# Performance work log

Hardware: AMD Instinct MI355X
Metric: run time of the kernel (lower is better)

The kernel has to match this reference:

```python
import jax, jax.numpy as jnp
import numpy as np

_CLIP_MIN = 1e-06
_POS_ALPHA = 0.001
NUM_CLASSES = 26
RADIUS = 3
POOL = 3  # rmi_pool_size == rmi_pool_stride
HALF_D = RADIUS * RADIUS


def _max_pool2d(x):
    # torch F.max_pool2d(kernel=3, stride=3, padding=1): pads with -inf
    return jax.lax.reduce_window(
        x, -jnp.inf, jax.lax.max,
        window_dimensions=(1, 1, POOL, POOL),
        window_strides=(1, 1, POOL, POOL),
        padding=[(0, 0), (0, 0), (1, 1), (1, 1)])


def _get_pairs(x):
    # stack radius^2 shifted views: [n,c,H,W] -> [n,c,half_d,new_h,new_w]
    h, w = x.shape[2], x.shape[3]
    nh, nw = h - (RADIUS - 1), w - (RADIUS - 1)
    views = [x[:, :, y:y + nh, xx:xx + nw] for y in range(RADIUS) for xx in range(RADIUS)]
    return jnp.stack(views, axis=2)


def _log_det_by_cholesky(m):
    chol = jnp.linalg.cholesky(m)
    diag = jnp.diagonal(chol, axis1=-2, axis2=-1)
    return 2.0 * jnp.sum(jnp.log(diag + 1e-08), axis=-1)


def _rmi_lower_bound(labels_4D, probs_4D):
    labels_4D = _max_pool2d(labels_4D)
    probs_4D = _max_pool2d(probs_4D)
    n, c = labels_4D.shape[0], labels_4D.shape[1]
    la = _get_pairs(labels_4D).reshape(n, c, HALF_D, -1)  # [n,c,9,M]
    pr = _get_pairs(probs_4D).reshape(n, c, HALF_D, -1)
    eye = jnp.eye(HALF_D, dtype=pr.dtype)
    la = la - jnp.mean(la, axis=3, keepdims=True)
    pr = pr - jnp.mean(pr, axis=3, keepdims=True)
    la_cov = jnp.einsum('ncdm,ncem->ncde', la, la)
    pr_cov = jnp.einsum('ncdm,ncem->ncde', pr, pr)
    pr_cov_inv = jnp.linalg.inv(pr_cov + eye * _POS_ALPHA)
    la_pr_cov = jnp.einsum('ncdm,ncem->ncde', la, pr)
    appro_var = la_cov - jnp.einsum('ncde,ncef,ncgf->ncdg', la_pr_cov, pr_cov_inv, la_pr_cov)
    rmi_now = 0.5 * _log_det_by_cholesky(appro_var + eye * _POS_ALPHA)  # [n,c]
    rmi_per_class = jnp.mean(rmi_now.reshape(-1, NUM_CLASSES), axis=0) / float(HALF_D)
    return jnp.sum(rmi_per_class)


def setup_inputs() -> dict:
    key = jax.random.key(0)
    k1, k2, k3 = jax.random.split(key, 3)
    n, c, h, w = 4, NUM_CLASSES, 512, 512
    cls_score = jax.random.normal(k1, (n, c, h, w), dtype=jnp.float32)
    new_targets = jax.random.randint(k2, (n, c, h, w), 0, 2).astype(jnp.float32)
    valid_indices = jax.random.randint(k3, (n, h, w), 0, 2).astype(jnp.float32)
    return {"cls_score": cls_score, "new_targets": new_targets, "valid_indices": valid_indices}


def reference(cls_score, new_targets, valid_indices):
    mask = valid_indices[:, None, :, :]  # [n,1,h,w]
    valid_onehot = new_targets * mask
    probs = jax.nn.sigmoid(cls_score) * mask + _CLIP_MIN
    return _rmi_lower_bound(valid_onehot, probs)
```

## Files before the change

kernel.cpp:

```cpp
#include <hip/hip_runtime.h>
#include <math.h>

#define NUM_CLASSES 26
#define HH 512
#define WW 512
#define NB 4
#define PHH 171
#define PWW 171
#define NHH 169
#define NWW 169
#define MPTS (NHH*NWW)
#define NCT (NB*NUM_CLASSES)
#define CLIPV 1e-6f
#define PSTR 176
#define NCHUNK 4
#define ROWS_PER_CHUNK 43
#define NSLOT 189

__global__ __launch_bounds__(256, 4) void pool_kernel(const float* __restrict__ cls,
        const float* __restrict__ tgt, const float* __restrict__ mask,
        float* __restrict__ poolL, float* __restrict__ poolP) {
    const int total = NCT * PHH * 43;
    for (int idx = blockIdx.x * 256 + threadIdx.x; idx < total; idx += gridDim.x * 256) {
        int t  = idx % 43;
        int rr = idx / 43;
        int ph = rr % PHH;
        int nc = rr / PHH;
        int n  = nc / NUM_CLASSES;

        const float* clsB = cls  + (size_t)nc * HH * WW;
        const float* tgtB = tgt  + (size_t)nc * HH * WW;
        const float* mB   = mask + (size_t)n  * HH * WW;

        float amax[16];
        #pragma unroll
        for (int i = 0; i < 16; ++i) amax[i] = -INFINITY;
        unsigned bbit = 0;

        const int f0 = (t == 0)  ? 1 : 0;
        const int f1 = (t == 42) ? 3 : 4;
        const int r0 = 3 * ph - 1;
        #pragma unroll
        for (int s = 0; s < 3; ++s) {
            int r = r0 + s;
            if (r < 0) continue;
            const float4* crow = (const float4*)(clsB + (size_t)r * WW) + (3 * t - 1);
            const float4* trow = (const float4*)(tgtB + (size_t)r * WW) + (3 * t - 1);
            const float4* mrow = (const float4*)(mB   + (size_t)r * WW) + (3 * t - 1);
            #pragma unroll
            for (int f = 0; f < 4; ++f) {
                if (f >= f0 && f < f1) {
                    float4 c = crow[f];
                    float4 g = trow[f];
                    float4 m = mrow[f];
                    float cc[4] = {c.x, c.y, c.z, c.w};
                    float gg[4] = {g.x, g.y, g.z, g.w};
                    float mm[4] = {m.x, m.y, m.z, m.w};
                    #pragma unroll
                    for (int k = 0; k < 4; ++k) {
                        int i = 4 * f + k;
                        amax[i] = fmaxf(amax[i], mm[k] > 0.5f ? cc[k] : -INFINITY);
                        bbit |= (gg[k] * mm[k] > 0.5f) ? (1u << i) : 0u;
                    }
                }
            }
        }
        float pout[4], lout[4];
        #pragma unroll
        for (int q = 0; q < 4; ++q) {
            float a = fmaxf(fmaxf(amax[3 * q + 3], amax[3 * q + 4]), amax[3 * q + 5]);
            int   b = (bbit >> (3 * q + 3)) & 7;
            pout[q] = __fdividef(1.0f, 1.0f + __expf(-a)) + CLIPV;
            lout[q] = b ? 1.0f : 0.0f;
        }
        size_t o = ((size_t)nc * PHH + ph) * PSTR + 4 * t;
        *(float4*)(poolP + o) = make_float4(pout[0], pout[1], pout[2], pout[3]);
        *(float4*)(poolL + o) = make_float4(lout[0], lout[1], lout[2], lout[3]);
        if (t == 42) {
            *(float4*)(poolP + o + 4) = make_float4(0.f, 0.f, 0.f, 0.f);
            *(float4*)(poolL + o + 4) = make_float4(0.f, 0.f, 0.f, 0.f);
        }
    }
}

__global__ __launch_bounds__(256, 3) void cov_kernel(const float* __restrict__ poolL,
        const float* __restrict__ poolP, float* __restrict__ partial) {
    const int nc = blockIdx.x, mode = blockIdx.y, ch = blockIdx.z;
    const int tid = threadIdx.x, lane = tid & 63, wave = tid >> 6;
    const int rowbase = ch * ROWS_PER_CHUNK;
    const int rc = (rowbase + ROWS_PER_CHUNK <= NHH) ? ROWS_PER_CHUNK : (NHH - rowbase);
    const float* Lb = poolL + (size_t)nc * PHH * PSTR;
    const float* Pb = poolP + (size_t)nc * PHH * PSTR;
    const int items = rc * 43;

    __shared__ float red[4][54];

    if (mode < 2) {
        const float* src = mode ? Pb : Lb;
        float acc[45], sm[9];
        #pragma unroll
        for (int k = 0; k < 45; ++k) acc[k] = 0.f;
        #pragma unroll
        for (int k = 0; k < 9; ++k) sm[k] = 0.f;

        for (int it = tid; it < items; it += 256) {
            int i  = rowbase + it / 43;
            int j0 = (it - (it / 43) * 43) * 4;
            const float* rp = src + (size_t)i * PSTR + j0;
            float4 x0 = *(const float4*)(rp);
            float4 x1 = *(const float4*)(rp + 4);
            float4 y0 = *(const float4*)(rp + PSTR);
            float4 y1 = *(const float4*)(rp + PSTR + 4);
            float4 z0 = *(const float4*)(rp + 2 * PSTR);
            float4 z1 = *(const float4*)(rp + 2 * PSTR + 4);
            float r0[8] = {x0.x, x0.y, x0.z, x0.w, x1.x, x1.y, x1.z, x1.w};
            float r1[8] = {y0.x, y0.y, y0.z, y0.w, y1.x, y1.y, y1.z, y1.w};
            float r2[8] = {z0.x, z0.y, z0.z, z0.w, z1.x, z1.y, z1.z, z1.w};
            #pragma unroll
            for (int q = 0; q < 4; ++q) {
                float sel = (j0 + q < NWW) ? 1.f : 0.f;
                float v[9], vs[9];
                v[0] = r0[q]; v[1] = r0[q + 1]; v[2] = r0[q + 2];
                v[3] = r1[q]; v[4] = r1[q + 1]; v[5] = r1[q + 2];
                v[6] = r2[q]; v[7] = r2[q + 1]; v[8] = r2[q + 2];
                #pragma unroll
                for (int d = 0; d < 9; ++d) { vs[d] = v[d] * sel; sm[d] += vs[d]; }
                int k = 0;
                #pragma unroll
                for (int d = 0; d < 9; ++d)
                    #pragma unroll
                    for (int e = d; e < 9; ++e)
                        acc[k++] += vs[d] * v[e];
            }
        }
        #pragma unroll
        for (int k = 0; k < 45; ++k) {
            float x = acc[k];
            #pragma unroll
            for (int off = 32; off > 0; off >>= 1) x += __shfl_down(x, off);
            if (lane == 0) red[wave][k] = x;
        }
        #pragma unroll
        for (int k = 0; k < 9; ++k) {
            float x = sm[k];
            #pragma unroll
            for (int off = 32; off > 0; off >>= 1) x += __shfl_down(x, off);
            if (lane == 0) red[wave][45 + k] = x;
        }
        __syncthreads();
        if (tid < 54) {
            float x = red[0][tid] + red[1][tid] + red[2][tid] + red[3][tid];
            int slot = (tid < 45) ? (mode == 0 ? 0 : 45) + tid
                                  : (mode == 0 ? 171 : 180) + (tid - 45);
            partial[((size_t)ch * NSLOT + slot) * NCT + nc] = x;
        }
    } else {
        const int nd  = (mode == 2) ? 5 : 4;
        const int dof = (mode == 2) ? 0 : 5;
        float acc[45];
        #pragma unroll
        for (int k = 0; k < 45; ++k) acc[k] = 0.f;

        for (int it = tid; it < items; it += 256) {
            int i  = rowbase + it / 43;
            int j0 = (it - (it / 43) * 43) * 4;
            const float* lp = Lb + (size_t)i * PSTR + j0;
            const float* pp = Pb + (size_t)i * PSTR + j0;
            float4 px0 = *(const float4*)(pp);
            float4 px1 = *(const float4*)(pp + 4);
            float4 py0 = *(const float4*)(pp + PSTR);
            float4 py1 = *(const float4*)(pp + PSTR + 4);
            float4 pz0 = *(const float4*)(pp + 2 * PSTR);
            float4 pz1 = *(const float4*)(pp + 2 * PSTR + 4);
            float pr0[8] = {px0.x, px0.y, px0.z, px0.w, px1.x, px1.y, px1.z, px1.w};
            float pr1[8] = {py0.x, py0.y, py0.z, py0.w, py1.x, py1.y, py1.z, py1.w};
            float pr2[8] = {pz0.x, pz0.y, pz0.z, pz0.w, pz1.x, pz1.y, pz1.z, pz1.w};
            const float* la = lp + (mode == 2 ? 0 : PSTR);
            const float* lb2 = lp + (mode == 2 ? PSTR : 2 * PSTR);
            float4 la0 = *(const float4*)(la);
            float4 la1 = *(const float4*)(la + 4);
            float4 lb0 = *(const float4*)(lb2);
            float4 lb1 = *(const float4*)(lb2 + 4);
            float lrA[8] = {la0.x, la0.y, la0.z, la0.w, la1.x, la1.y, la1.z, la1.w};
            float lrB[8] = {lb0.x, lb0.y, lb0.z, lb0.w, lb1.x, lb1.y, lb1.z, lb1.w};
            #pragma unroll
            for (int q = 0; q < 4; ++q) {
                float sel = (j0 + q < NWW) ? 1.f : 0.f;
                float vp[9];
                vp[0] = pr0[q]; vp[1] = pr0[q + 1]; vp[2] = pr0[q + 2];
                vp[3] = pr1[q]; vp[4] = pr1[q + 1]; vp[5] = pr1[q + 2];
                vp[6] = pr2[q]; vp[7] = pr2[q + 1]; vp[8] = pr2[q + 2];
                float vl[5];
                if (mode == 2) {
                    vl[0] = lrA[q] * sel; vl[1] = lrA[q + 1] * sel; vl[2] = lrA[q + 2] * sel;
                    vl[3] = lrB[q] * sel; vl[4] = lrB[q + 1] * sel;
                } else {
                    vl[0] = lrA[q + 2] * sel;
                    vl[1] = lrB[q] * sel; vl[2] = lrB[q + 1] * sel; vl[3] = lrB[q + 2] * sel;
                }
                #pragma unroll
                for (int d = 0; d < 5; ++d) {
                    if (d < nd) {
                        #pragma unroll
                        for (int e = 0; e < 9; ++e)
                            acc[d * 9 + e] += vl[d] * vp[e];
                    }
                }
            }
        }
        const int nred = nd * 9;
        #pragma unroll
        for (int k = 0; k < 45; ++k) {
            if (k < nred) {
                float x = acc[k];
                #pragma unroll
                for (int off = 32; off > 0; off >>= 1) x += __shfl_down(x, off);
                if (lane == 0) red[wave][k] = x;
            }
        }
        __syncthreads();
        if (tid < nred) {
            float x = red[0][tid] + red[1][tid] + red[2][tid] + red[3][tid];
            int slot = 90 + (dof * 9) + tid;
            partial[((size_t)ch * NSLOT + slot) * NCT + nc] = x;
        }
    }
}

__global__ __launch_bounds__(128) void solve_kernel(const float* __restrict__ partial,
                                                    double* __restrict__ per_nc) {
    const int nc = blockIdx.x;
    const int tid = threadIdx.x;
    __shared__ double cl[45], cp[45], clp[81], sL[9], sP[9];
    __shared__ double All[81], C[81], Pm[81], X[81], A[81];
    __shared__ double logacc;

    for (int s = tid; s < NSLOT; s += 128) {
        double acc = 0.0;
        for (int ch = 0; ch < NCHUNK; ++ch)
            acc += (double)partial[((size_t)ch * NSLOT + s) * NCT + nc];
        if (s < 45)       cl[s] = acc;
        else if (s < 90)  cp[s - 45] = acc;
        else if (s < 171) clp[s - 90] = acc;
        else if (s < 180) sL[s - 171] = acc;
        else              sP[s - 180] = acc;
    }
    if (tid == 0) logacc = 0.0;
    __syncthreads();

    const double M = (double)MPTS;
    if (tid < 81) {
        int d = tid / 9, e = tid % 9;
        int lo = d < e ? d : e, hi = d < e ? e : d;
        int k = 9 * lo - lo * (lo - 1) / 2 + (hi - lo);
        All[tid] = cl[k] - sL[d] * sL[e] / M;
        C[tid]   = cp[k] - sP[d] * sP[e] / M + (d == e ? 1e-3 : 0.0);
        Pm[tid]  = clp[tid] - sL[d] * sP[e] / M;
    }
    __syncthreads();

    for (int k = 0; k < 9; ++k) {
        if (tid == 0) C[k * 9 + k] = sqrt(fmax(C[k * 9 + k], 1e-30));
        __syncthreads();
        if (tid > k && tid < 9) C[tid * 9 + k] /= C[k * 9 + k];
        __syncthreads();
        if (tid < 81) {
            int i = tid / 9, j = tid % 9;
            if (j > k && i >= j) C[i * 9 + j] -= C[i * 9 + k] * C[j * 9 + k];
        }
        __syncthreads();
    }

    for (int e = 0; e < 9; ++e) {
        if (tid < 9) {
            int d = tid;
            double sum = Pm[d * 9 + e];
            for (int k = 0; k < e; ++k) sum -= C[e * 9 + k] * X[k * 9 + d];
            X[e * 9 + d] = sum / C[e * 9 + e];
        }
        __syncthreads();
    }

    if (tid < 81) {
        int d = tid / 9, g = tid % 9;
        double w = 0.0;
        #pragma unroll
        for (int e = 0; e < 9; ++e) w += X[e * 9 + d] * X[e * 9 + g];
        A[tid] = All[tid] - w + (d == g ? 1e-3 : 0.0);
    }
    __syncthreads();

    for (int k = 0; k < 9; ++k) {
        if (tid == 0) {
            double piv = sqrt(fmax(A[k * 9 + k], 0.0));
            A[k * 9 + k] = piv;
            logacc += log(piv + 1e-8);
        }
        __syncthreads();
        if (tid > k && tid < 9) A[tid * 9 + k] /= A[k * 9 + k];
        __syncthreads();
        if (tid < 81) {
            int i = tid / 9, j = tid % 9;
            if (j > k && i >= j) A[i * 9 + j] -= A[i * 9 + k] * A[j * 9 + k];
        }
        __syncthreads();
    }
    if (tid == 0) per_nc[nc] = logacc;
}

__global__ __launch_bounds__(128) void reduce_kernel(const double* __restrict__ per_nc,
                                                     float* __restrict__ out) {
    int t = threadIdx.x;
    double r = (t < NCT) ? per_nc[t] : 0.0;
    __shared__ double red[128];
    red[t] = r;
    __syncthreads();
    for (int s = 64; s > 0; s >>= 1) {
        if (t < s) red[t] += red[t + s];
        __syncthreads();
    }
    if (t == 0) out[0] = (float)(red[0] / 36.0);
}

extern "C" void kernel_launch(void* const* d_in, const int* in_sizes, int n_in,
                              void* d_out, int out_size, void* d_ws, size_t ws_size,
                              hipStream_t stream) {
    const float* cls  = (const float*)d_in[0];
    const float* tgt  = (const float*)d_in[1];
    const float* mask = (const float*)d_in[2];

    double* per_nc  = (double*)d_ws;
    float*  poolL   = (float*)(per_nc + 128);
    float*  poolP   = poolL + (size_t)NCT * PHH * PSTR;
    float*  partial = poolP + (size_t)NCT * PHH * PSTR;

    pool_kernel<<<1024, 256, 0, stream>>>(cls, tgt, mask, poolL, poolP);

    dim3 gcov(NCT, 4, NCHUNK);
    cov_kernel<<<gcov, 256, 0, stream>>>(poolL, poolP, partial);

    solve_kernel<<<NCT, 128, 0, stream>>>(partial, per_nc);

    reduce_kernel<<<1, 128, 0, stream>>>(per_nc, (float*)d_out);
}
```

Baseline: 323.1 us.

## Restructure pooling to one wave per pooled row and split covariance into more chunks

```diff
diff --git a/kernel.cpp b/kernel.cpp
--- a/kernel.cpp
+++ b/kernel.cpp
@@ -13,77 +13,77 @@
 #define NCT (NB*NUM_CLASSES)
 #define CLIPV 1e-6f
 #define PSTR 176
-#define NCHUNK 4
-#define ROWS_PER_CHUNK 43
+#define NCHUNK 8
+#define ROWS_PER_CHUNK 22
 #define NSLOT 189
 
-__global__ __launch_bounds__(256, 4) void pool_kernel(const float* __restrict__ cls,
+__global__ __launch_bounds__(256) void pool_kernel(const float* __restrict__ cls,
         const float* __restrict__ tgt, const float* __restrict__ mask,
         float* __restrict__ poolL, float* __restrict__ poolP) {
-    const int total = NCT * PHH * 43;
-    for (int idx = blockIdx.x * 256 + threadIdx.x; idx < total; idx += gridDim.x * 256) {
-        int t  = idx % 43;
-        int rr = idx / 43;
-        int ph = rr % PHH;
-        int nc = rr / PHH;
-        int n  = nc / NUM_CLASSES;
-
-        const float* clsB = cls  + (size_t)nc * HH * WW;
-        const float* tgtB = tgt  + (size_t)nc * HH * WW;
-        const float* mB   = mask + (size_t)n  * HH * WW;
-
-        float amax[16];
-        #pragma unroll
-        for (int i = 0; i < 16; ++i) amax[i] = -INFINITY;
-        unsigned bbit = 0;
-
-        const int f0 = (t == 0)  ? 1 : 0;
-        const int f1 = (t == 42) ? 3 : 4;
-        const int r0 = 3 * ph - 1;
-        #pragma unroll
-        for (int s = 0; s < 3; ++s) {
-            int r = r0 + s;
-            if (r < 0) continue;
-            const float4* crow = (const float4*)(clsB + (size_t)r * WW) + (3 * t - 1);
-            const float4* trow = (const float4*)(tgtB + (size_t)r * WW) + (3 * t - 1);
-            const float4* mrow = (const float4*)(mB   + (size_t)r * WW) + (3 * t - 1);
-            #pragma unroll
-            for (int f = 0; f < 4; ++f) {
-                if (f >= f0 && f < f1) {
-                    float4 c = crow[f];
-                    float4 g = trow[f];
-                    float4 m = mrow[f];
-                    float cc[4] = {c.x, c.y, c.z, c.w};
-                    float gg[4] = {g.x, g.y, g.z, g.w};
-                    float mm[4] = {m.x, m.y, m.z, m.w};
-                    #pragma unroll
-                    for (int k = 0; k < 4; ++k) {
-                        int i = 4 * f + k;
-                        amax[i] = fmaxf(amax[i], mm[k] > 0.5f ? cc[k] : -INFINITY);
-                        bbit |= (gg[k] * mm[k] > 0.5f) ? (1u << i) : 0u;
-                    }
-                }
-            }
-        }
-        float pout[4], lout[4];
-        #pragma unroll
-        for (int q = 0; q < 4; ++q) {
-            float a = fmaxf(fmaxf(amax[3 * q + 3], amax[3 * q + 4]), amax[3 * q + 5]);
-            int   b = (bbit >> (3 * q + 3)) & 7;
-            pout[q] = __fdividef(1.0f, 1.0f + __expf(-a)) + CLIPV;
-            lout[q] = b ? 1.0f : 0.0f;
-        }
-        size_t o = ((size_t)nc * PHH + ph) * PSTR + 4 * t;
-        *(float4*)(poolP + o) = make_float4(pout[0], pout[1], pout[2], pout[3]);
-        *(float4*)(poolL + o) = make_float4(lout[0], lout[1], lout[2], lout[3]);
-        if (t == 42) {
-            *(float4*)(poolP + o + 4) = make_float4(0.f, 0.f, 0.f, 0.f);
-            *(float4*)(poolL + o + 4) = make_float4(0.f, 0.f, 0.f, 0.f);
-        }
-    }
-}
-
-__global__ __launch_bounds__(256, 3) void cov_kernel(const float* __restrict__ poolL,
+    __shared__ float amax[4][512];
+    __shared__ float lmax[4][512];
+    const int w = threadIdx.x >> 6, lane = threadIdx.x & 63;
+    const int R = blockIdx.x * 4 + w;
+    const int ph = R % PHH, nc = R / PHH, n = nc / NUM_CLASSES;
+
+    const float4* c4 = (const float4*)(cls  + (size_t)nc * HH * WW);
+    const float4* t4 = (const float4*)(tgt  + (size_t)nc * HH * WW);
+    const float4* m4 = (const float4*)(mask + (size_t)n  * HH * WW);
+
+    float am[8], lm[8];
+    #pragma unroll
+    for (int k = 0; k < 8; ++k) { am[k] = -INFINITY; lm[k] = 0.f; }
+
+    const int r0 = 3 * ph - 1;
+    const int s0 = (ph == 0) ? 1 : 0;
+    for (int s = s0; s < 3; ++s) {
+        int rbase = (r0 + s) * 128;
+        #pragma unroll
+        for (int g = 0; g < 2; ++g) {
+            int i4 = rbase + lane + 64 * g;
+            float4 c = c4[i4];
+            float4 t = t4[i4];
+            float4 m = m4[i4];
+            float cc[4] = {c.x, c.y, c.z, c.w};
+            float tt[4] = {t.x, t.y, t.z, t.w};
+            float mm[4] = {m.x, m.y, m.z, m.w};
+            #pragma unroll
+            for (int k = 0; k < 4; ++k) {
+                int j = 4 * g + k;
+                am[j] = fmaxf(am[j], mm[k] > 0.5f ? cc[k] : -INFINITY);
+                lm[j] = fmaxf(lm[j], tt[k] * mm[k]);
+            }
+        }
+    }
+    *(float4*)&amax[w][4 * lane]       = make_float4(am[0], am[1], am[2], am[3]);
+    *(float4*)&amax[w][256 + 4 * lane] = make_float4(am[4], am[5], am[6], am[7]);
+    *(float4*)&lmax[w][4 * lane]       = make_float4(lm[0], lm[1], lm[2], lm[3]);
+    *(float4*)&lmax[w][256 + 4 * lane] = make_float4(lm[4], lm[5], lm[6], lm[7]);
+    __syncthreads();
+
+    const size_t rowo = (size_t)(nc * PHH + ph) * PSTR;
+    #pragma unroll
+    for (int j = 0; j < 3; ++j) {
+        int pw = lane + 64 * j;
+        if (pw < PWW) {
+            int cM = 3 * pw;
+            float a = fmaxf(amax[w][cM], amax[w][cM + 1]);
+            float l = fmaxf(lmax[w][cM], lmax[w][cM + 1]);
+            if (cM > 0) {
+                a = fmaxf(a, amax[w][cM - 1]);
+                l = fmaxf(l, lmax[w][cM - 1]);
+            }
+            poolP[rowo + pw] = __fdividef(1.0f, 1.0f + __expf(-a)) + CLIPV;
+            poolL[rowo + pw] = (l > 0.5f) ? 1.0f : 0.0f;
+        } else if (j == 2 && lane >= 43 && lane < 48) {
+            int pc = 128 + lane;
+            poolP[rowo + pc] = 0.f;
+            poolL[rowo + pc] = 0.f;
+        }
+    }
+}
+
+__global__ __launch_bounds__(256, 4) void cov_kernel(const float* __restrict__ poolL,
         const float* __restrict__ poolP, float* __restrict__ partial) {
     const int nc = blockIdx.x, mode = blockIdx.y, ch = blockIdx.z;
     const int tid = threadIdx.x, lane = tid & 63, wave = tid >> 6;
@@ -175,7 +175,7 @@
             float pr0[8] = {px0.x, px0.y, px0.z, px0.w, px1.x, px1.y, px1.z, px1.w};
             float pr1[8] = {py0.x, py0.y, py0.z, py0.w, py1.x, py1.y, py1.z, py1.w};
             float pr2[8] = {pz0.x, pz0.y, pz0.z, pz0.w, pz1.x, pz1.y, pz1.z, pz1.w};
-            const float* la = lp + (mode == 2 ? 0 : PSTR);
+            const float* la  = lp + (mode == 2 ? 0 : PSTR);
             const float* lb2 = lp + (mode == 2 ? PSTR : 2 * PSTR);
             float4 la0 = *(const float4*)(la);
             float4 la1 = *(const float4*)(la + 4);
@@ -334,7 +334,7 @@
     float*  poolP   = poolL + (size_t)NCT * PHH * PSTR;
     float*  partial = poolP + (size_t)NCT * PHH * PSTR;
 
-    pool_kernel<<<1024, 256, 0, stream>>>(cls, tgt, mask, poolL, poolP);
+    pool_kernel<<<NCT * PHH / 4, 256, 0, stream>>>(cls, tgt, mask, poolL, poolP);
 
     dim3 gcov(NCT, 4, NCHUNK);
     cov_kernel<<<gcov, 256, 0, stream>>>(poolL, poolP, partial);
```

Measured after the change: 316.6 us. -2.0%, faster.
